# Kernel tuning notes

Measured on AMD Instinct MI355X. Metric: run time of the kernel, lower is better.

## Reference

```python
import jax, jax.numpy as jnp
import numpy as np

B = 2097152          # number of query points (e.g. one per pixel of a ~1448^2 image)
N_CTRL = 62          # N_ctrl_pts from __init__
GRID = N_CTRL + 2    # control grid size = 64
MASK_B = 1           # maskBoundary
A = -0.75            # PyTorch bicubic convolution coefficient


def _cubic_weights(t):
    # Weights of the Keys cubic kernel (a=-0.75) for taps at offsets (-1,0,1,2).
    # t in [0,1) is the fractional coordinate. Shapes: t [b] -> [b,4].
    s = 1.0 - t
    w0 = A * t * s * s                      # cc2(t+1)
    w1 = (A + 2.0) * t**3 - (A + 3.0) * t**2 + 1.0   # cc1(t)
    w2 = (A + 2.0) * s**3 - (A + 3.0) * s**2 + 1.0   # cc1(1-t)
    w3 = A * s * t * t                      # cc2(2-t)
    return jnp.stack([w0, w1, w2, w3], axis=-1)


def _reflect(idx, size):
    # PyTorch reflection padding with align_corners=True: reflect about 0 and size-1.
    period = 2 * (size - 1)
    idx = jnp.abs(idx) % period
    return jnp.where(idx >= size, period - idx, idx)


def _bicubic_sample(img, coordinate):
    # img: [c, H, W] (same for every query); coordinate: [b, 2] as (y, x) in [-1,1].
    # Equivalent to: affine_grid(theta, size=(b,c,1,1), align_corners=True) +
    # grid_sample(mode='bicubic', padding_mode='reflection', align_corners=True)
    # where theta = [[1/H, 0, x], [0, 1/H, y]] -> single sample at (x-1/H, y-1/H).
    c, H, W = img.shape
    crop = 1.0 / H
    gx = coordinate[:, 1] - crop   # grid x indexes width
    gy = coordinate[:, 0] - crop   # grid y indexes height
    ix = (gx + 1.0) * 0.5 * (W - 1)   # unnormalize, align_corners=True
    iy = (gy + 1.0) * 0.5 * (H - 1)
    ix0 = jnp.floor(ix)
    iy0 = jnp.floor(iy)
    tx = ix - ix0                      # fractional parts (differentiable wrt coords)
    ty = iy - iy0
    offs = jnp.arange(-1, 3, dtype=jnp.int32)
    xs = jnp.clip(_reflect(ix0.astype(jnp.int32)[:, None] + offs, W), 0, W - 1)  # [b,4]
    ys = jnp.clip(_reflect(iy0.astype(jnp.int32)[:, None] + offs, H), 0, H - 1)  # [b,4]
    wx = _cubic_weights(tx)  # [b,4]
    wy = _cubic_weights(ty)  # [b,4]
    # gather 4x4 neighborhoods: vals[c,b,i,j] = img[c, ys[b,i], xs[b,j]]
    vals = img[:, ys[:, :, None], xs[:, None, :]]  # [c, b, 4, 4]
    return jnp.einsum('cbij,bi,bj->bc', vals, wy, wx)  # [b, c]


def _forward(coordinate, depl_ctr_pts, mask):
    img = depl_ctr_pts * mask          # masked control-point displacement field [2,H,W]
    return _bicubic_sample(img, coordinate)  # [b, 2] (torch.squeeze of [b,2,1,1])


def setup_inputs() -> dict:
    key = jax.random.key(0)
    k1, k2 = jax.random.split(key)
    max_ampl = 1.0 / (N_CTRL - 1)
    depl = (jax.random.uniform(k1, (2, GRID, GRID), jnp.float32) - 0.5) * 2.0 * max_ampl
    border = jnp.zeros((GRID,), bool).at[:MASK_B].set(True).at[-MASK_B:].set(True)
    bm = border[:, None] | border[None, :]
    mask = jnp.where(bm[None, :, :], 0.0, jnp.ones((2, GRID, GRID), jnp.float32))
    depl = depl * mask  # __init__ zeros the boundary ring of the stored param too
    coordinate = jax.random.uniform(k2, (B, 2), jnp.float32, minval=-1.0, maxval=1.0)
    return {"coordinate": coordinate, "depl_ctr_pts": depl, "mask": mask}


def reference(coordinate, depl_ctr_pts, mask):
    return _forward(coordinate, depl_ctr_pts, mask)
```

## Files before the change

kernel.cpp:

```cpp
#include <hip/hip_runtime.h>
#include <hip/hip_fp16.h>

#define TPB 256
#define MAXGRID 2048

#define PW 68

__device__ __forceinline__ void cubic_w(float t, float w[4]) {
    float s = 1.0f - t;
    float t2 = t * t;
    float s2 = s * s;
    w[0] = -0.75f * t * s2;
    w[1] = 1.25f * (t2 * t) - 2.25f * t2 + 1.0f;
    w[2] = 1.25f * (s2 * s) - 2.25f * s2 + 1.0f;
    w[3] = -0.75f * s * t2;
}

__global__ __launch_bounds__(TPB, 8) void deformation_field_kernel(
        const float2* __restrict__ coord2,
        const float4* __restrict__ depl4,
        const float4* __restrict__ mask4,
        float2* __restrict__ out2,
        int n_pts)
{
    __shared__ __half2 img[PW * PW];

    for (int i = threadIdx.x; i < 1024; i += TPB) {
        float4 d0 = depl4[i];
        float4 m0 = mask4[i];
        float4 d1 = depl4[1024 + i];
        float4 m1 = mask4[1024 + i];
        int o = i * 4;
        int r = o >> 6;
        int c = o & 63;
        int pb = (r + 2) * PW + (c + 2);
        img[pb + 0] = __floats2half2_rn(d0.x * m0.x, d1.x * m1.x);
        img[pb + 1] = __floats2half2_rn(d0.y * m0.y, d1.y * m1.y);
        img[pb + 2] = __floats2half2_rn(d0.z * m0.z, d1.z * m1.z);
        img[pb + 3] = __floats2half2_rn(d0.w * m0.w, d1.w * m1.w);
    }
    __syncthreads();

    {
        int t = threadIdx.x;
        int r = 2 + (t & 63);
        int j = t >> 6;
        int sel = j & 1, half = j >> 1;
        int dc = half ? (66 + sel) : sel;
        int sc = half ? (64 - sel) : (4 - sel);
        img[r * PW + dc] = img[r * PW + sc];
    }
    __syncthreads();

    if (threadIdx.x < PW) {
        int c = threadIdx.x;
        img[0 * PW + c]  = img[4 * PW + c];
        img[1 * PW + c]  = img[3 * PW + c];
        img[66 * PW + c] = img[64 * PW + c];
        img[67 * PW + c] = img[63 * PW + c];
    }
    __syncthreads();

    const int stride = gridDim.x * TPB;
    int p = blockIdx.x * TPB + threadIdx.x;
    if (p >= n_pts) return;

    float2 c = coord2[p];
    for (;;) {
        int pn = p + stride;
        bool has = (pn < n_pts);
        float2 cn;
        if (has) cn = coord2[pn];

        float ix = fmaf(c.y, 31.5f, 31.0078125f);
        float iy = fmaf(c.x, 31.5f, 31.0078125f);
        float fx = floorf(ix);
        float fy = floorf(iy);
        float tx = ix - fx;
        float ty = iy - fy;
        int jx = (int)fx;
        int jy = (int)fy;

        float wx[4], wy[4];
        cubic_w(tx, wx);
        cubic_w(ty, wy);
        __half2 wxh[4];
        #pragma unroll
        for (int k = 0; k < 4; ++k) wxh[k] = __float2half2_rn(wx[k]);

        int base = (jy + 1) * PW + (jx + 1);

        float a0 = 0.0f, a1 = 0.0f;
        #pragma unroll
        for (int i = 0; i < 4; ++i) {
            int rb = base + i * PW;
            __half2 r = __hmul2(wxh[0], img[rb + 0]);
            r = __hfma2(wxh[1], img[rb + 1], r);
            r = __hfma2(wxh[2], img[rb + 2], r);
            r = __hfma2(wxh[3], img[rb + 3], r);
            a0 = fmaf(wy[i], __low2float(r), a0);
            a1 = fmaf(wy[i], __high2float(r), a1);
        }
        out2[p] = make_float2(a0, a1);

        if (!has) break;
        p = pn;
        c = cn;
    }
}

extern "C" void kernel_launch(void* const* d_in, const int* in_sizes, int n_in,
                              void* d_out, int out_size, void* d_ws, size_t ws_size,
                              hipStream_t stream) {
    const float2* coord2 = (const float2*)d_in[0];
    const float4* depl4  = (const float4*)d_in[1];
    const float4* mask4  = (const float4*)d_in[2];
    float2* out2 = (float2*)d_out;

    int n_pts = in_sizes[0] / 2;
    int grid = (n_pts + TPB - 1) / TPB;
    if (grid > MAXGRID) grid = MAXGRID;
    if (grid < 1) grid = 1;

    deformation_field_kernel<<<grid, TPB, 0, stream>>>(coord2, depl4, mask4, out2, n_pts);
}
```

Before: 79.36 us.

## Add shifted LDS image copy for 8-byte aligned tap loads, use 1024-thread blocks

Keeps a second copy of the padded half2 image in LDS, shifted by one element. Each 4-tap row can then be read with two aligned 64-bit LDS loads instead of four 32-bit loads, with odd x offsets served from the shifted copy. Blocks grow to 1024 threads with a grid capped at 512, so the per-block prologue now runs over fewer, larger blocks. LDS use doubles and there is an extra copy pass plus barrier before sampling, which could reduce occupancy.

Result: faster. 76.02 us (-4.2%).

```diff
diff --git a/kernel.cpp b/kernel.cpp
--- a/kernel.cpp
+++ b/kernel.cpp
@@ -1,10 +1,12 @@
 #include <hip/hip_runtime.h>
 #include <hip/hip_fp16.h>
 
-#define TPB 256
-#define MAXGRID 2048
+#define TPB 1024
+#define MAXGRID 512
 
 #define PW 68
+#define NPAD (PW * PW)
+#define OFFB NPAD
 
 __device__ __forceinline__ void cubic_w(float t, float w[4]) {
     float s = 1.0f - t;
@@ -23,9 +25,12 @@
         float2* __restrict__ out2,
         int n_pts)
 {
-    __shared__ __half2 img[PW * PW];
+    __shared__ __half2 img[2 * NPAD];
 
-    for (int i = threadIdx.x; i < 1024; i += TPB) {
+    const int tid = threadIdx.x;
+
+    {
+        int i = tid;
         float4 d0 = depl4[i];
         float4 m0 = mask4[i];
         float4 d1 = depl4[1024 + i];
@@ -41,10 +46,9 @@
     }
     __syncthreads();
 
-    {
-        int t = threadIdx.x;
-        int r = 2 + (t & 63);
-        int j = t >> 6;
+    if (tid < 256) {
+        int r = 2 + (tid & 63);
+        int j = tid >> 6;
         int sel = j & 1, half = j >> 1;
         int dc = half ? (66 + sel) : sel;
         int sc = half ? (64 - sel) : (4 - sel);
@@ -52,17 +56,21 @@
     }
     __syncthreads();
 
-    if (threadIdx.x < PW) {
-        int c = threadIdx.x;
-        img[0 * PW + c]  = img[4 * PW + c];
-        img[1 * PW + c]  = img[3 * PW + c];
-        img[66 * PW + c] = img[64 * PW + c];
-        img[67 * PW + c] = img[63 * PW + c];
+    if (tid < 4 * PW) {
+        int j = tid / PW;
+        int c = tid - j * PW;
+        int dr = (j & 2) ? (66 + (j & 1)) : (j & 1);
+        int sr = (j & 2) ? (64 - (j & 1)) : (4 - (j & 1));
+        img[dr * PW + c] = img[sr * PW + c];
     }
     __syncthreads();
 
+    for (int d = tid; d < NPAD - 1; d += TPB)
+        img[OFFB + d] = img[d + 1];
+    __syncthreads();
+
     const int stride = gridDim.x * TPB;
-    int p = blockIdx.x * TPB + threadIdx.x;
+    int p = blockIdx.x * TPB + tid;
     if (p >= n_pts) return;
 
     float2 c = coord2[p];
@@ -78,8 +86,8 @@
         float fy = floorf(iy);
         float tx = ix - fx;
         float ty = iy - fy;
-        int jx = (int)fx;
-        int jy = (int)fy;
+        int jxp = (int)fx + 1;
+        int jyp = (int)fy + 1;
 
         float wx[4], wy[4];
         cubic_w(tx, wx);
@@ -88,16 +96,22 @@
         #pragma unroll
         for (int k = 0; k < 4; ++k) wxh[k] = __float2half2_rn(wx[k]);
 
-        int base = (jy + 1) * PW + (jx + 1);
+        int dbase = jyp * PW + (jxp & ~1) + ((jxp & 1) ? OFFB : 0);
+        const __half2* bp = &img[dbase];
 
         float a0 = 0.0f, a1 = 0.0f;
         #pragma unroll
         for (int i = 0; i < 4; ++i) {
-            int rb = base + i * PW;
-            __half2 r = __hmul2(wxh[0], img[rb + 0]);
-            r = __hfma2(wxh[1], img[rb + 1], r);
-            r = __hfma2(wxh[2], img[rb + 2], r);
-            r = __hfma2(wxh[3], img[rb + 3], r);
+            uint2 ua = *reinterpret_cast<const uint2*>(bp + i * PW);
+            uint2 ub = *reinterpret_cast<const uint2*>(bp + i * PW + 2);
+            __half2 t0 = *reinterpret_cast<const __half2*>(&ua.x);
+            __half2 t1 = *reinterpret_cast<const __half2*>(&ua.y);
+            __half2 t2 = *reinterpret_cast<const __half2*>(&ub.x);
+            __half2 t3 = *reinterpret_cast<const __half2*>(&ub.y);
+            __half2 r = __hmul2(wxh[0], t0);
+            r = __hfma2(wxh[1], t1, r);
+            r = __hfma2(wxh[2], t2, r);
+            r = __hfma2(wxh[3], t3, r);
             a0 = fmaf(wy[i], __low2float(r), a0);
             a1 = fmaf(wy[i], __high2float(r), a1);
         }
```
